# Kernel optimization log

Hardware: AMD Instinct MI355X
Metric: run time of the kernel (lower is better)

Reference implementation:

```python
import jax, jax.numpy as jnp
import numpy as np

N = 50000      # nodes
E = 800000     # edges
IN, HID, OUT = 256, 256, 128
FCH = 32       # fc_hidden per embedding
VDIM = 2
FINAL = 2
NUM_EMB = 20


def setup_inputs() -> dict:
    key = jax.random.key(0)
    ks = jax.random.split(key, 16)
    s = 0.05
    return {
        "x": jax.random.normal(ks[0], (N, IN), jnp.float32),
        "edge_index": jax.random.randint(ks[1], (2, E), 0, N),
        "edge_cat": jax.random.randint(ks[2], (E, 2), 0, NUM_EMB),
        "edge_val": jax.random.normal(ks[3], (E, VDIM), jnp.float32),
        "W1": jax.random.normal(ks[4], (IN, HID), jnp.float32) * s,
        "b1": jnp.zeros((HID,), jnp.float32),
        "W2": jax.random.normal(ks[5], (HID, OUT), jnp.float32) * s,
        "b2": jnp.zeros((OUT,), jnp.float32),
        "emb0": jax.random.normal(ks[6], (NUM_EMB, FCH), jnp.float32) * s,
        "emb1": jax.random.normal(ks[7], (NUM_EMB, FCH), jnp.float32) * s,
        "fW1": jax.random.normal(ks[8], (OUT + 2 * FCH + VDIM, FINAL), jnp.float32) * s,
        "fb1": jnp.zeros((FINAL,), jnp.float32),
        "fW2": jax.random.normal(ks[9], (FINAL, 2), jnp.float32) * s,
        "fb2": jnp.zeros((2,), jnp.float32),
    }


def gcn_conv(h_in, W, b, src, dst, n):
    # PyG GCNConv: linear, add self-loops, symmetric D^-1/2 (A+I) D^-1/2 aggregation, bias.
    h = h_in @ W                                    # [N, F]
    ones = jnp.ones(src.shape[0], h.dtype)
    deg = jax.ops.segment_sum(ones, dst, num_segments=n) + 1.0  # +1 self-loop
    dinv = jax.lax.rsqrt(deg)                       # deg >= 1 so finite
    norm = dinv[src] * dinv[dst]                    # [E]
    agg = jax.ops.segment_sum(h[src] * norm[:, None], dst, num_segments=n)
    agg = agg + h * (dinv * dinv)[:, None]          # self-loop term, norm = dinv_i^2
    return agg + b


def reference(x, edge_index, edge_cat, edge_val,
              W1, b1, W2, b2, emb0, emb1, fW1, fb1, fW2, fb2):
    src, dst = edge_index[0], edge_index[1]
    n = x.shape[0]
    h = jax.nn.relu(gcn_conv(x, W1, b1, src, dst, n))
    h = gcn_conv(h, W2, b2, src, dst, n)            # [N, OUT]
    node2edge = h[src] - h[dst]                     # [E, OUT]
    ev = jnp.concatenate([edge_val, emb0[edge_cat[:, 0]], emb1[edge_cat[:, 1]]], axis=1)
    total = jnp.concatenate([node2edge, ev], axis=1)  # [E, OUT+2*FCH+VDIM]
    z = jax.nn.relu(total @ fW1 + fb1)              # dropout is identity in eval mode
    return z @ fW2 + fb2                            # [E, 2]
```

## Files before the change

### kernel.cpp

```cpp
#include <hip/hip_runtime.h>

#define NN 50000
#define XPAD 50048
#define EE 800000
#define NB ((NN + 1023) / 1024)
#define DEGB ((EE + 255) / 256)
#define NCVT (XPAD / 16)
#define GEMMB (2 * (XPAD / 64))

typedef _Float16 half8v __attribute__((ext_vector_type(8)));
typedef _Float16 half4v __attribute__((ext_vector_type(4)));
typedef float f32x4 __attribute__((ext_vector_type(4)));

__device__ __forceinline__ void gload16(const _Float16* g, _Float16* l) {
    __builtin_amdgcn_global_load_lds(
        (const __attribute__((address_space(1))) unsigned int*)g,
        (__attribute__((address_space(3))) unsigned int*)l, 16, 0, 0);
}

__global__ __launch_bounds__(256) void deg_prep(const int* __restrict__ dst,
                                                int* __restrict__ deg,
                                                int* __restrict__ epos,
                                                const float* __restrict__ x,
                                                _Float16* __restrict__ xh,
                                                const float* __restrict__ W1,
                                                const float* __restrict__ W2,
                                                const float* __restrict__ fW1,
                                                const float* __restrict__ emb0,
                                                const float* __restrict__ emb1,
                                                _Float16* __restrict__ BT,
                                                float* __restrict__ Wft,
                                                float2* __restrict__ t0,
                                                float2* __restrict__ t1) {
    __shared__ float T[64][65];
    int b = blockIdx.x;
    int t = threadIdx.x;
    if (b < DEGB) {
        int e = b * 256 + t;
        if (e < EE) epos[e] = atomicAdd(&deg[dst[e]], 1);
    } else if (b < DEGB + NCVT) {
        int b2 = b - DEGB;
        int row = b2 * 16 + (t >> 4);
        int col = (t & 15) * 16;
        half8v h0, h1;
        if (row < NN) {
            const float4* xp = (const float4*)&x[(size_t)row * 256 + col];
            float4 v0 = xp[0], v1 = xp[1], v2 = xp[2], v3 = xp[3];
            h0[0] = (_Float16)v0.x; h0[1] = (_Float16)v0.y;
            h0[2] = (_Float16)v0.z; h0[3] = (_Float16)v0.w;
            h0[4] = (_Float16)v1.x; h0[5] = (_Float16)v1.y;
            h0[6] = (_Float16)v1.z; h0[7] = (_Float16)v1.w;
            h1[0] = (_Float16)v2.x; h1[1] = (_Float16)v2.y;
            h1[2] = (_Float16)v2.z; h1[3] = (_Float16)v2.w;
            h1[4] = (_Float16)v3.x; h1[5] = (_Float16)v3.y;
            h1[6] = (_Float16)v3.z; h1[7] = (_Float16)v3.w;
        } else {
            h0 = (half8v)(_Float16)0.f;
            h1 = (half8v)(_Float16)0.f;
        }
        *(half8v*)&xh[(size_t)row * 256 + col] = h0;
        *(half8v*)&xh[(size_t)row * 256 + col + 8] = h1;
    } else if (b < DEGB + NCVT + 16) {
        int bb = b - DEGB - NCVT;
        int k0 = (bb >> 2) * 64, n0 = (bb & 3) * 64;
#pragma unroll
        for (int i = 0; i < 16; ++i) {
            int r = i * 4 + (t >> 6), c = t & 63;
            T[r][c] = W1[(size_t)(k0 + r) * 256 + n0 + c];
        }
        __syncthreads();
#pragma unroll
        for (int i = 0; i < 16; ++i) {
            int n = i * 4 + (t >> 6), k = t & 63;
            BT[(size_t)(n0 + n) * 256 + k0 + k] = (_Float16)T[k][n];
        }
    } else {
        int k = t;
        float s0 = 0.f, s1 = 0.f;
        for (int m = 0; m < 128; ++m) {
            float wv = W2[(size_t)k * 128 + m];
            s0 += wv * fW1[m * 2 + 0];
            s1 += wv * fW1[m * 2 + 1];
        }
        Wft[k] = s0;
        Wft[256 + k] = s1;
        if (k < 20) {
            float a0 = 0.f, a1 = 0.f, b0 = 0.f, b1v = 0.f;
            for (int u = 0; u < 32; ++u) {
                float e0 = emb0[k * 32 + u], e1 = emb1[k * 32 + u];
                a0 += e0 * fW1[(130 + u) * 2 + 0];
                a1 += e0 * fW1[(130 + u) * 2 + 1];
                b0 += e1 * fW1[(162 + u) * 2 + 0];
                b1v += e1 * fW1[(162 + u) * 2 + 1];
            }
            t0[k] = make_float2(a0, a1);
            t1[k] = make_float2(b0, b1v);
        }
    }
}

__global__ __launch_bounds__(1024) void scan_partial(const int* __restrict__ deg,
                                                     int* __restrict__ rowptr,
                                                     int* __restrict__ bsum) {
    __shared__ int wsum[16];
    int tid = threadIdx.x, lane = tid & 63, w = tid >> 6;
    int idx = blockIdx.x * 1024 + tid;
    int v = (idx < NN) ? deg[idx] : 0;
    int x = v;
#pragma unroll
    for (int off = 1; off < 64; off <<= 1) {
        int t = __shfl_up(x, off, 64);
        if (lane >= off) x += t;
    }
    if (lane == 63) wsum[w] = x;
    __syncthreads();
    if (w == 0) {
        int s = (lane < 16) ? wsum[lane] : 0;
#pragma unroll
        for (int off = 1; off < 16; off <<= 1) {
            int t = __shfl_up(s, off, 64);
            if (lane >= off) s += t;
        }
        if (lane < 16) wsum[lane] = s;
    }
    __syncthreads();
    int wpre = (w == 0) ? 0 : wsum[w - 1];
    if (idx < NN) rowptr[idx] = wpre + (x - v);
    if (tid == 0) bsum[blockIdx.x] = wsum[15];
}

__global__ __launch_bounds__(256) void scan_add_dinv(int* __restrict__ rowptr,
                                                     const int* __restrict__ bsum,
                                                     const int* __restrict__ deg,
                                                     float* __restrict__ dinv) {
    __shared__ int pre[NB + 1];
    int t = threadIdx.x;
    if (t < 64) {
        int v = (t < NB) ? bsum[t] : 0;
        int x = v;
#pragma unroll
        for (int o = 1; o < 64; o <<= 1) {
            int y = __shfl_up(x, o, 64);
            if (t >= o) x += y;
        }
        if (t < NB) pre[t] = x - v;
        if (t == NB - 1) pre[NB] = x;
    }
    __syncthreads();
    int idx = blockIdx.x * 256 + t;
    if (idx < NN) {
        rowptr[idx] += pre[idx >> 10];
        dinv[idx] = rsqrtf((float)deg[idx] + 1.0f);
    }
    if (blockIdx.x == 0 && t == 0) rowptr[NN] = pre[NB];
}

__global__ __launch_bounds__(256) void gemm_fill(const _Float16* __restrict__ Axh,
                                                 const _Float16* __restrict__ BT,
                                                 _Float16* __restrict__ C, int M,
                                                 const int* __restrict__ src,
                                                 const int* __restrict__ dst,
                                                 const int* __restrict__ rowptr,
                                                 const int* __restrict__ epos,
                                                 int* __restrict__ csr_src) {
    if (blockIdx.x >= GEMMB) {
        int e = (blockIdx.x - GEMMB) * 256 + threadIdx.x;
        if (e < EE) {
            int d = dst[e];
            csr_src[rowptr[d] + epos[e]] = src[e];
        }
        return;
    }
    __shared__ _Float16 Ah[64 * 32];
    __shared__ _Float16 Bh[128 * 32];
    int tid = threadIdx.x;
    int bm = (blockIdx.x >> 1) * 64, bn = (blockIdx.x & 1) * 128;
    int w = tid >> 6, l = tid & 63;
    int wr = w >> 1, wc = w & 1;
    int lr = l & 15, lg = l >> 4;
    const _Float16* gA = Axh + (size_t)(bm + (tid >> 2)) * 256 + (tid & 3) * 8;
    const _Float16* gB0 = BT + (size_t)(bn + (tid >> 2)) * 256 + (tid & 3) * 8;
    const _Float16* gB1 = BT + (size_t)(bn + ((tid + 256) >> 2)) * 256 + (tid & 3) * 8;
    _Float16* lA = Ah + tid * 8;
    _Float16* lB0 = Bh + tid * 8;
    _Float16* lB1 = Bh + (tid + 256) * 8;
    f32x4 acc[2][4] = {};

#pragma unroll
    for (int ks = 0; ks < 8; ++ks) {
        int k0 = ks * 32;
        gload16(gA + k0, lA);
        gload16(gB0 + k0, lB0);
        gload16(gB1 + k0, lB1);
        __syncthreads();
        half8v a[2], b[4];
#pragma unroll
        for (int mf = 0; mf < 2; ++mf)
            a[mf] = *(const half8v*)&Ah[(wr * 32 + mf * 16 + lr) * 32 + lg * 8];
#pragma unroll
        for (int nf = 0; nf < 4; ++nf)
            b[nf] = *(const half8v*)&Bh[(wc * 64 + nf * 16 + lr) * 32 + lg * 8];
#pragma unroll
        for (int mf = 0; mf < 2; ++mf)
#pragma unroll
            for (int nf = 0; nf < 4; ++nf)
                acc[mf][nf] = __builtin_amdgcn_mfma_f32_16x16x32_f16(a[mf], b[nf], acc[mf][nf], 0, 0, 0);
        if (ks < 7) __syncthreads();
    }
#pragma unroll
    for (int mf = 0; mf < 2; ++mf) {
#pragma unroll
        for (int reg = 0; reg < 4; ++reg) {
            int gr = bm + wr * 32 + mf * 16 + lg * 4 + reg;
            if (gr < M) {
#pragma unroll
                for (int nf = 0; nf < 4; ++nf)
                    C[(size_t)gr * 256 + bn + wc * 64 + nf * 16 + lr] =
                        (_Float16)acc[mf][nf][reg];
            }
        }
    }
}

__global__ __launch_bounds__(256) void gather_project(const _Float16* __restrict__ hs,
                                                      const int* __restrict__ rowptr,
                                                      const int* __restrict__ csr_src,
                                                      const float* __restrict__ dinv,
                                                      const float* __restrict__ b1,
                                                      const float* __restrict__ Wft,
                                                      float2* __restrict__ q) {
    int i = blockIdx.x * 4 + (threadIdx.x >> 6);
    int l = threadIdx.x & 63;
    int lf = l & 31, le = l >> 5;
    if (i >= NN) return;
    int start = rowptr[i], end = rowptr[i + 1];
    float acc[8] = {};
    int j = start;
    for (; j + 7 < end; j += 8) {
        int s0 = csr_src[j + 0 + le];
        int s1 = csr_src[j + 2 + le];
        int s2 = csr_src[j + 4 + le];
        int s3 = csr_src[j + 6 + le];
        float d0 = dinv[s0], d1 = dinv[s1], d2 = dinv[s2], d3 = dinv[s3];
        half8v v0 = *(const half8v*)(hs + (size_t)s0 * 256 + lf * 8);
        half8v v1 = *(const half8v*)(hs + (size_t)s1 * 256 + lf * 8);
        half8v v2 = *(const half8v*)(hs + (size_t)s2 * 256 + lf * 8);
        half8v v3 = *(const half8v*)(hs + (size_t)s3 * 256 + lf * 8);
#pragma unroll
        for (int u = 0; u < 8; ++u)
            acc[u] += (d0 * (float)v0[u] + d1 * (float)v1[u]) +
                      (d2 * (float)v2[u] + d3 * (float)v3[u]);
    }
    for (; j + le < end; j += 2) {
        int s = csr_src[j + le];
        float ds = dinv[s];
        half8v v = *(const half8v*)(hs + (size_t)s * 256 + lf * 8);
#pragma unroll
        for (int u = 0; u < 8; ++u) acc[u] += ds * (float)v[u];
    }
#pragma unroll
    for (int u = 0; u < 8; ++u) acc[u] += __shfl_xor(acc[u], 32, 64);
    float di = dinv[i];
    half8v sv = *(const half8v*)(hs + (size_t)i * 256 + lf * 8);
    float q0 = 0.f, q1 = 0.f;
#pragma unroll
    for (int u = 0; u < 8; ++u) {
        float o = fmaxf((acc[u] + di * (float)sv[u]) * di + b1[lf * 8 + u], 0.f);
        q0 += o * Wft[lf * 8 + u];
        q1 += o * Wft[256 + lf * 8 + u];
    }
#pragma unroll
    for (int off = 16; off > 0; off >>= 1) {
        q0 += __shfl_xor(q0, off, 64);
        q1 += __shfl_xor(q1, off, 64);
    }
    if (l == 0) q[i] = make_float2(q0 * di, q1 * di);
}

__global__ __launch_bounds__(256) void gather_gn(const float2* __restrict__ q,
                                                 const int* __restrict__ rowptr,
                                                 const int* __restrict__ csr_src,
                                                 const float* __restrict__ dinv,
                                                 float2* __restrict__ gn) {
    int i = blockIdx.x * blockDim.x + threadIdx.x;
    if (i >= NN) return;
    int start = rowptr[i], end = rowptr[i + 1];
    float a0 = 0.f, a1 = 0.f;
    for (int j = start; j < end; ++j) {
        float2 v = q[csr_src[j]];
        a0 += v.x;
        a1 += v.y;
    }
    float2 self = q[i];
    float di = dinv[i];
    gn[i] = make_float2((a0 + self.x) * di, (a1 + self.y) * di);
}

__global__ __launch_bounds__(256) void edge_out(const float2* __restrict__ gn,
                                                const int* __restrict__ src,
                                                const int* __restrict__ dst,
                                                const int2* __restrict__ ecat,
                                                const float2* __restrict__ ev,
                                                const float* __restrict__ fW1,
                                                const float2* __restrict__ t0,
                                                const float2* __restrict__ t1,
                                                const float* __restrict__ fb1,
                                                const float* __restrict__ fW2,
                                                const float* __restrict__ fb2,
                                                float2* __restrict__ out) {
    int e = blockIdx.x * blockDim.x + threadIdx.x;
    if (e >= EE) return;
    int s = src[e], d = dst[e];
    float2 gs = gn[s], gd = gn[d];
    int2 c = ecat[e];
    float2 v = ev[e];
    float2 e0 = t0[c.x], e1 = t1[c.y];
    float z0 = gs.x - gd.x + v.x * fW1[128 * 2 + 0] + v.y * fW1[129 * 2 + 0] + e0.x + e1.x;
    float z1 = gs.y - gd.y + v.x * fW1[128 * 2 + 1] + v.y * fW1[129 * 2 + 1] + e0.y + e1.y;
    float y0 = fmaxf(z0 + fb1[0], 0.f);
    float y1 = fmaxf(z1 + fb1[1], 0.f);
    out[e] = make_float2(y0 * fW2[0] + y1 * fW2[2] + fb2[0],
                         y0 * fW2[1] + y1 * fW2[3] + fb2[1]);
}

extern "C" void kernel_launch(void* const* d_in, const int* in_sizes, int n_in,
                              void* d_out, int out_size, void* d_ws, size_t ws_size,
                              hipStream_t stream) {
    const float* x    = (const float*)d_in[0];
    const int*   eidx = (const int*)d_in[1];
    const int*   src  = eidx;
    const int*   dst  = eidx + EE;
    const int*   ecat = (const int*)d_in[2];
    const float* ev   = (const float*)d_in[3];
    const float* W1   = (const float*)d_in[4];
    const float* b1   = (const float*)d_in[5];
    const float* W2   = (const float*)d_in[6];
    const float* emb0 = (const float*)d_in[8];
    const float* emb1 = (const float*)d_in[9];
    const float* fW1  = (const float*)d_in[10];
    const float* fb1  = (const float*)d_in[11];
    const float* fW2  = (const float*)d_in[12];
    const float* fb2  = (const float*)d_in[13];
    float* out = (float*)d_out;

    char* ws = (char*)d_ws;
    size_t off = 0;
    auto alloc = [&](size_t bytes) {
        void* p = ws + off;
        off = (off + bytes + 255) & ~(size_t)255;
        return p;
    };
    int*      deg     = (int*)alloc((size_t)NN * 4);
    float*    dinv    = (float*)alloc((size_t)NN * 4);
    int*      rowptr  = (int*)alloc((size_t)(NN + 1) * 4);
    int*      bsum    = (int*)alloc((size_t)NB * 4);
    int*      epos    = (int*)alloc((size_t)EE * 4);
    int*      csr_src = (int*)alloc((size_t)EE * 4);
    _Float16* W1T     = (_Float16*)alloc((size_t)256 * 256 * 2);
    _Float16* xh      = (_Float16*)alloc((size_t)XPAD * 256 * 2);
    _Float16* h1s     = (_Float16*)alloc((size_t)NN * 256 * 2);
    float2*   q       = (float2*)alloc((size_t)NN * 8);
    float2*   gn      = (float2*)alloc((size_t)NN * 8);
    float*    Wft     = (float*)alloc(512 * 4);
    float2*   t0      = (float2*)alloc(20 * 8);
    float2*   t1      = (float2*)alloc(20 * 8);

    hipMemsetAsync(deg, 0, (size_t)NN * 4, stream);

    deg_prep<<<DEGB + NCVT + 17, 256, 0, stream>>>(dst, deg, epos, x, xh,
                                                   W1, W2, fW1, emb0, emb1,
                                                   W1T, Wft, t0, t1);

    scan_partial<<<NB, 1024, 0, stream>>>(deg, rowptr, bsum);
    scan_add_dinv<<<(NN + 255) / 256, 256, 0, stream>>>(rowptr, bsum, deg, dinv);

    gemm_fill<<<GEMMB + DEGB, 256, 0, stream>>>(xh, W1T, h1s, NN,
                                                src, dst, rowptr, epos, csr_src);

    gather_project<<<(NN + 3) / 4, 256, 0, stream>>>(
        h1s, rowptr, csr_src, dinv, b1, Wft, q);
    gather_gn<<<(NN + 255) / 256, 256, 0, stream>>>(q, rowptr, csr_src, dinv, gn);
    edge_out<<<DEGB, 256, 0, stream>>>(
        gn, src, dst, (const int2*)ecat, (const float2*)ev,
        fW1, t0, t1, fb1, fW2, fb2, (float2*)out);
}
```

Before: 165.0 us.

## Double-buffer GEMM LDS loads and widen tile to full 256 output columns

The GEMM kernel now uses 512-thread blocks that each compute a 64x256 output tile, so every A tile is loaded once instead of twice. LDS is double-buffered so the next K-slice is issued before the MFMAs on the current slice, which overlaps load latency with compute. The CSR fill path moves to 512 threads per block to match. This doubles LDS use per block and may lower occupancy, and the async global_load_lds issued to the other buffer relies on the single barrier per iteration for correctness.

```diff
diff --git a/kernel.cpp b/kernel.cpp
--- a/kernel.cpp
+++ b/kernel.cpp
@@ -6,7 +6,8 @@
 #define NB ((NN + 1023) / 1024)
 #define DEGB ((EE + 255) / 256)
 #define NCVT (XPAD / 16)
-#define GEMMB (2 * (XPAD / 64))
+#define GEMMB (XPAD / 64)
+#define FILLB ((EE + 511) / 512)
 
 typedef _Float16 half8v __attribute__((ext_vector_type(8)));
 typedef _Float16 half4v __attribute__((ext_vector_type(4)));
@@ -155,7 +156,7 @@
     if (blockIdx.x == 0 && t == 0) rowptr[NN] = pre[NB];
 }
 
-__global__ __launch_bounds__(256) void gemm_fill(const _Float16* __restrict__ Axh,
+__global__ __launch_bounds__(512) void gemm_fill(const _Float16* __restrict__ Axh,
                                                  const _Float16* __restrict__ BT,
                                                  _Float16* __restrict__ C, int M,
                                                  const int* __restrict__ src,
@@ -164,48 +165,51 @@
                                                  const int* __restrict__ epos,
                                                  int* __restrict__ csr_src) {
     if (blockIdx.x >= GEMMB) {
-        int e = (blockIdx.x - GEMMB) * 256 + threadIdx.x;
+        int e = (blockIdx.x - GEMMB) * 512 + threadIdx.x;
         if (e < EE) {
             int d = dst[e];
             csr_src[rowptr[d] + epos[e]] = src[e];
         }
         return;
     }
-    __shared__ _Float16 Ah[64 * 32];
-    __shared__ _Float16 Bh[128 * 32];
+    __shared__ _Float16 Ah[2][64 * 32];
+    __shared__ _Float16 Bh[2][256 * 32];
     int tid = threadIdx.x;
-    int bm = (blockIdx.x >> 1) * 64, bn = (blockIdx.x & 1) * 128;
+    int bm = blockIdx.x * 64;
     int w = tid >> 6, l = tid & 63;
-    int wr = w >> 1, wc = w & 1;
+    int wr = w >> 2, wc = w & 3;
     int lr = l & 15, lg = l >> 4;
-    const _Float16* gA = Axh + (size_t)(bm + (tid >> 2)) * 256 + (tid & 3) * 8;
-    const _Float16* gB0 = BT + (size_t)(bn + (tid >> 2)) * 256 + (tid & 3) * 8;
-    const _Float16* gB1 = BT + (size_t)(bn + ((tid + 256) >> 2)) * 256 + (tid & 3) * 8;
-    _Float16* lA = Ah + tid * 8;
-    _Float16* lB0 = Bh + tid * 8;
-    _Float16* lB1 = Bh + (tid + 256) * 8;
     f32x4 acc[2][4] = {};
 
+    const _Float16* gA  = Axh + (size_t)(bm + (tid >> 2)) * 256 + (tid & 3) * 8;
+    const _Float16* gB0 = BT + (size_t)(tid >> 2) * 256 + (tid & 3) * 8;
+    const _Float16* gB1 = BT + (size_t)((tid >> 2) + 128) * 256 + (tid & 3) * 8;
+
+    auto stage = [&](int buf, int k0) {
+        if (tid < 256) gload16(gA + k0, &Ah[buf][tid * 8]);
+        gload16(gB0 + k0, &Bh[buf][tid * 8]);
+        gload16(gB1 + k0, &Bh[buf][(tid + 512) * 8]);
+    };
+
+    stage(0, 0);
+    __syncthreads();
 #pragma unroll
     for (int ks = 0; ks < 8; ++ks) {
-        int k0 = ks * 32;
-        gload16(gA + k0, lA);
-        gload16(gB0 + k0, lB0);
-        gload16(gB1 + k0, lB1);
-        __syncthreads();
+        int cur = ks & 1;
+        if (ks < 7) stage(cur ^ 1, (ks + 1) * 32);
         half8v a[2], b[4];
 #pragma unroll
         for (int mf = 0; mf < 2; ++mf)
-            a[mf] = *(const half8v*)&Ah[(wr * 32 + mf * 16 + lr) * 32 + lg * 8];
+            a[mf] = *(const half8v*)&Ah[cur][(wr * 32 + mf * 16 + lr) * 32 + lg * 8];
 #pragma unroll
         for (int nf = 0; nf < 4; ++nf)
-            b[nf] = *(const half8v*)&Bh[(wc * 64 + nf * 16 + lr) * 32 + lg * 8];
+            b[nf] = *(const half8v*)&Bh[cur][(wc * 64 + nf * 16 + lr) * 32 + lg * 8];
 #pragma unroll
         for (int mf = 0; mf < 2; ++mf)
 #pragma unroll
             for (int nf = 0; nf < 4; ++nf)
                 acc[mf][nf] = __builtin_amdgcn_mfma_f32_16x16x32_f16(a[mf], b[nf], acc[mf][nf], 0, 0, 0);
-        if (ks < 7) __syncthreads();
+        __syncthreads();
     }
 #pragma unroll
     for (int mf = 0; mf < 2; ++mf) {
@@ -215,7 +219,7 @@
             if (gr < M) {
 #pragma unroll
                 for (int nf = 0; nf < 4; ++nf)
-                    C[(size_t)gr * 256 + bn + wc * 64 + nf * 16 + lr] =
+                    C[(size_t)gr * 256 + wc * 64 + nf * 16 + lr] =
                         (_Float16)acc[mf][nf][reg];
             }
         }
@@ -374,8 +378,8 @@
     scan_partial<<<NB, 1024, 0, stream>>>(deg, rowptr, bsum);
     scan_add_dinv<<<(NN + 255) / 256, 256, 0, stream>>>(rowptr, bsum, deg, dinv);
 
-    gemm_fill<<<GEMMB + DEGB, 256, 0, stream>>>(xh, W1T, h1s, NN,
-                                                src, dst, rowptr, epos, csr_src);
+    gemm_fill<<<GEMMB + FILLB, 512, 0, stream>>>(xh, W1T, h1s, NN,
+                                                 src, dst, rowptr, epos, csr_src);
 
     gather_project<<<(NN + 3) / 4, 256, 0, stream>>>(
         h1s, rowptr, csr_src, dinv, b1, Wft, q);
```

After: 164.0 us. No clear change (-0.6%).
